# Kernel optimization log

Hardware: AMD Instinct MI355X
Metric: run time of the kernel (lower is better)

Reference implementation:

```python
import jax, jax.numpy as jnp
import numpy as np


def setup_inputs() -> dict:
    key = jax.random.key(0)
    ks = jax.random.split(key, 6)
    B, S, H, F, E = 4, 2048, 1024, 4096, 8
    x = jax.random.normal(ks[0], (B, S, H), dtype=jnp.float32)
    Wg = jax.random.normal(ks[1], (H, E), dtype=jnp.float32) * (1.0 / np.sqrt(H))
    W1 = jax.random.normal(ks[2], (E, H, F), dtype=jnp.float32) * (1.0 / np.sqrt(H))
    b1 = jnp.zeros((E, F), dtype=jnp.float32)
    W2 = jax.random.normal(ks[3], (E, F, H), dtype=jnp.float32) * (1.0 / np.sqrt(F))
    b2 = jnp.zeros((E, H), dtype=jnp.float32)
    return {"x": x, "Wg": Wg, "W1": W1, "b1": b1, "W2": W2, "b2": b2}


def _moe_forward(x, Wg, W1, b1, W2, b2):
    B, S, H = x.shape
    E = Wg.shape[1]
    tokens = x.reshape(-1, H)            # [T, H]
    T = tokens.shape[0]
    C = -(-T // E)                       # capacity = ceil(T/E), capacity_factor=1.0, min_capacity=0

    # --- top-1 gating (deepspeed top1gating) ---
    logits = tokens @ Wg                 # [T, E]
    gates = jax.nn.softmax(logits, axis=-1)
    idx = jnp.argmax(gates, axis=1)      # chosen expert per token
    mask1 = jax.nn.one_hot(idx, E, dtype=gates.dtype)          # [T, E]
    locations1 = jnp.cumsum(mask1, axis=0) - 1.0               # position within expert
    mask1 = mask1 * (locations1 < C).astype(gates.dtype)       # drop tokens over capacity
    loc_s = jnp.sum(locations1 * mask1, axis=1).astype(jnp.int32)  # [T]
    gates1 = jnp.sum(gates * mask1, axis=1)                    # [T] gate value (0 if dropped)

    # dispatch mask [T, E, C]: 1 at (token's expert, token's slot) if kept
    loc_oh = jax.nn.one_hot(loc_s, C, dtype=gates.dtype)       # [T, C]
    dispatch = mask1[:, :, None] * loc_oh[:, None, :]          # [T, E, C]
    combine = gates1[:, None, None] * dispatch                 # [T, E, C]

    # --- dispatch -> grouped expert MLP -> combine ---
    expert_in = jnp.einsum("tec,th->ech", dispatch, tokens)    # [E, C, H]
    hidden = jax.nn.relu(jnp.einsum("ech,ehf->ecf", expert_in, W1) + b1[:, None, :])
    expert_out = jnp.einsum("ecf,efh->ech", hidden, W2) + b2[:, None, :]
    out = jnp.einsum("tec,ech->th", combine, expert_out)       # [T, H]
    return out.reshape(B, S, H)


def reference(x, Wg, W1, b1, W2, b2):
    return _moe_forward(x, Wg, W1, b1, W2, b2)
```

## Files before the change

### kernel.cpp

```cpp
#include <hip/hip_runtime.h>
#include <hip/hip_bf16.h>
#include <hip/hip_fp16.h>

#define T_TOK 8192
#define HDIM  1024
#define FDIM  4096
#define NEXP  8
#define CAP   1024

typedef _Float16 f16x8 __attribute__((ext_vector_type(8)));
typedef float    f32x4 __attribute__((ext_vector_type(4)));

__device__ __forceinline__ unsigned short f2h_u(float f) {
    _Float16 h = (_Float16)f;
    return __builtin_bit_cast(unsigned short, h);
}

#define GLOAD_LDS16(gp, lp)                                                              \
    __builtin_amdgcn_global_load_lds((const __attribute__((address_space(1))) void*)(gp),\
                                     (__attribute__((address_space(3))) void*)(lp),      \
                                     16, 0, 0)

__global__ __launch_bounds__(256) void gate_kernel(const float* __restrict__ x,
                                                   const float* __restrict__ Wg,
                                                   int* __restrict__ eidx,
                                                   float* __restrict__ gate) {
    __shared__ float wgt[NEXP * HDIM];
    const int tid = threadIdx.x;
    for (int i = tid; i < NEXP * HDIM; i += 256) {
        int h = i >> 3, e = i & 7;
        wgt[e * HDIM + h] = Wg[i];
    }
    __syncthreads();
    const int lane = tid & 63;
    const int t = blockIdx.x * 4 + (tid >> 6);
    const float* xr = x + (size_t)t * HDIM;
    float acc[NEXP];
#pragma unroll
    for (int e = 0; e < NEXP; e++) acc[e] = 0.f;
    for (int h = lane; h < HDIM; h += 64) {
        float xv = xr[h];
#pragma unroll
        for (int e = 0; e < NEXP; e++) acc[e] += xv * wgt[e * HDIM + h];
    }
#pragma unroll
    for (int e = 0; e < NEXP; e++) {
#pragma unroll
        for (int s = 32; s > 0; s >>= 1) acc[e] += __shfl_xor(acc[e], s);
    }
    if (lane == 0) {
        float mx = acc[0]; int mi = 0;
#pragma unroll
        for (int e = 1; e < NEXP; e++) { if (acc[e] > mx) { mx = acc[e]; mi = e; } }
        float den = 0.f;
#pragma unroll
        for (int e = 0; e < NEXP; e++) den += expf(acc[e] - mx);
        eidx[t] = mi;
        gate[t] = 1.0f / den;
    }
}

__global__ __launch_bounds__(512) void scan_kernel(const int* __restrict__ eidx,
                                                   const float* __restrict__ gate,
                                                   int* __restrict__ tok,
                                                   float* __restrict__ gslot) {
    __shared__ int sidx[T_TOK];
    for (int i = threadIdx.x; i < T_TOK; i += 512) sidx[i] = eidx[i];
    __syncthreads();
    const int e = threadIdx.x >> 6, lane = threadIdx.x & 63;
    const unsigned long long below = (lane == 0) ? 0ull : (~0ull >> (64 - lane));
    int cnt = 0;
    for (int c0 = 0; c0 < T_TOK; c0 += 64) {
        int t = c0 + lane;
        int my = sidx[t];
        unsigned long long b = __ballot(my == e);
        if (my == e) {
            int pos = cnt + __popcll(b & below);
            if (pos < CAP) { tok[e * CAP + pos] = t; gslot[e * CAP + pos] = gate[t]; }
        }
        cnt += __popcll(b);
    }
}

__global__ __launch_bounds__(256) void gather_kernel(const float* __restrict__ x,
                                                     const int* __restrict__ tok,
                                                     unsigned short* __restrict__ A) {
    const int row = blockIdx.x;
    const int t = tok[row];
    unsigned short* dst = A + (size_t)row * HDIM;
    if (t < 0) {
        ushort4 z; z.x = z.y = z.z = z.w = 0;
        ((ushort4*)dst)[threadIdx.x] = z;
    } else {
        float4 v = ((const float4*)(x + (size_t)t * HDIM))[threadIdx.x];
        ushort4 o;
        o.x = f2h_u(v.x); o.y = f2h_u(v.y); o.z = f2h_u(v.z); o.w = f2h_u(v.w);
        ((ushort4*)dst)[threadIdx.x] = o;
    }
}

__global__ __launch_bounds__(256) void transpose_kernel(const float* __restrict__ in,
                                                        unsigned short* __restrict__ out,
                                                        int R, int Cdim) {
    __shared__ unsigned short tile[64][72];
    const int e = blockIdx.z;
    const size_t esz = (size_t)R * Cdim;
    const float* ine = in + e * esz;
    unsigned short* oute = out + e * esz;
    const int r0 = blockIdx.y * 64, c0 = blockIdx.x * 64;
    const int tid = threadIdx.x;
    const int rr = tid >> 4;
    const int c4 = (tid & 15) * 4;
#pragma unroll
    for (int rb = 0; rb < 64; rb += 16) {
        int r = rb + rr;
        float4 v = *(const float4*)&ine[(size_t)(r0 + r) * Cdim + c0 + c4];
        tile[c4 + 0][r] = f2h_u(v.x);
        tile[c4 + 1][r] = f2h_u(v.y);
        tile[c4 + 2][r] = f2h_u(v.z);
        tile[c4 + 3][r] = f2h_u(v.w);
    }
    __syncthreads();
    const int c = tid >> 2;
    const int rseg = (tid & 3) * 16;
    ushort4 o0 = *(const ushort4*)&tile[c][rseg + 0];
    ushort4 o1 = *(const ushort4*)&tile[c][rseg + 4];
    ushort4 o2 = *(const ushort4*)&tile[c][rseg + 8];
    ushort4 o3 = *(const ushort4*)&tile[c][rseg + 12];
    unsigned short* op = &oute[(size_t)(c0 + c) * R + r0 + rseg];
    ((ushort4*)op)[0] = o0; ((ushort4*)op)[1] = o1;
    ((ushort4*)op)[2] = o2; ((ushort4*)op)[3] = o3;
}

__global__ __launch_bounds__(256) void gemm1_kernel(const unsigned short* __restrict__ A,
                                                    const unsigned short* __restrict__ Bt,
                                                    const float* __restrict__ b1,
                                                    unsigned short* __restrict__ hid) {
    __shared__ __align__(16) unsigned short As[128 * 64];
    __shared__ __align__(16) unsigned short Bs[128 * 64];
    const int e = blockIdx.z;
    const int m0 = blockIdx.y * 128;
    const int n0 = blockIdx.x * 128;
    const int tid = threadIdx.x;
    const int lane = tid & 63;
    const int wr = ((tid >> 7) & 1) * 64;
    const int wc = ((tid >> 6) & 1) * 64;
    const unsigned short* Ae = A + ((size_t)e * CAP + m0) * HDIM;
    const unsigned short* Be = Bt + ((size_t)e * FDIM + n0) * HDIM;
    f32x4 acc[4][4];
    f32x4 zz = {0.f, 0.f, 0.f, 0.f};
#pragma unroll
    for (int i = 0; i < 4; i++)
#pragma unroll
        for (int j = 0; j < 4; j++) acc[i][j] = zz;

    const int srow = tid >> 3;
    const int sslot = tid & 7;
    for (int k0 = 0; k0 < HDIM; k0 += 64) {
#pragma unroll
        for (int j = 0; j < 4; j++) {
            int row = j * 32 + srow;
            int col = k0 + ((sslot ^ (row & 7)) << 3);
            GLOAD_LDS16(Ae + (size_t)row * HDIM + col, &As[(size_t)(j * 256 + tid) * 8]);
            GLOAD_LDS16(Be + (size_t)row * HDIM + col, &Bs[(size_t)(j * 256 + tid) * 8]);
        }
        __syncthreads();
#pragma unroll
        for (int ks = 0; ks < 2; ks++) {
            f16x8 af[4], bfr[4];
#pragma unroll
            for (int mi = 0; mi < 4; mi++) {
                int row = wr + mi * 16 + (lane & 15);
                int slotk = ks * 4 + (lane >> 4);
                af[mi] = *(const f16x8*)((const char*)As + row * 128 + ((slotk ^ (row & 7)) << 4));
            }
#pragma unroll
            for (int ni = 0; ni < 4; ni++) {
                int row = wc + ni * 16 + (lane & 15);
                int slotk = ks * 4 + (lane >> 4);
                bfr[ni] = *(const f16x8*)((const char*)Bs + row * 128 + ((slotk ^ (row & 7)) << 4));
            }
#pragma unroll
            for (int mi = 0; mi < 4; mi++)
#pragma unroll
                for (int ni = 0; ni < 4; ni++)
                    acc[mi][ni] = __builtin_amdgcn_mfma_f32_16x16x32_f16(af[mi], bfr[ni], acc[mi][ni], 0, 0, 0);
        }
        __syncthreads();
    }
    const int r4 = (lane >> 4) * 4;
#pragma unroll
    for (int ni = 0; ni < 4; ni++) {
        int col = n0 + wc + ni * 16 + (lane & 15);
        float bv = b1[e * FDIM + col];
#pragma unroll
        for (int mi = 0; mi < 4; mi++) {
#pragma unroll
            for (int j = 0; j < 4; j++) {
                int row = m0 + wr + mi * 16 + r4 + j;
                float v = acc[mi][ni][j] + bv;
                hid[((size_t)e * CAP + row) * FDIM + col] = f2h_u(v > 0.f ? v : 0.f);
            }
        }
    }
}

__global__ __launch_bounds__(256) void gemm2_kernel(const unsigned short* __restrict__ A,
                                                    const unsigned short* __restrict__ Bt,
                                                    const float* __restrict__ b2,
                                                    const int* __restrict__ tok,
                                                    const float* __restrict__ gslot,
                                                    float* __restrict__ out) {
    __shared__ __align__(16) unsigned short As[128 * 64];
    __shared__ __align__(16) unsigned short Bs[128 * 64];
    __shared__ int ts[128];
    __shared__ float sg[128];
    const int e = blockIdx.z;
    const int m0 = blockIdx.y * 128;
    const int n0 = blockIdx.x * 128;
    const int tid = threadIdx.x;
    if (tid < 128) {
        int t = tok[e * CAP + m0 + tid];
        ts[tid] = t;
        sg[tid] = (t >= 0) ? gslot[e * CAP + m0 + tid] : 0.f;
    }
    const int lane = tid & 63;
    const int wr = ((tid >> 7) & 1) * 64;
    const int wc = ((tid >> 6) & 1) * 64;
    const unsigned short* Ae = A + ((size_t)e * CAP + m0) * FDIM;
    const unsigned short* Be = Bt + ((size_t)e * HDIM + n0) * FDIM;
    f32x4 acc[4][4];
    f32x4 zz = {0.f, 0.f, 0.f, 0.f};
#pragma unroll
    for (int i = 0; i < 4; i++)
#pragma unroll
        for (int j = 0; j < 4; j++) acc[i][j] = zz;

    const int srow = tid >> 3;
    const int sslot = tid & 7;
    for (int k0 = 0; k0 < FDIM; k0 += 64) {
#pragma unroll
        for (int j = 0; j < 4; j++) {
            int row = j * 32 + srow;
            int col = k0 + ((sslot ^ (row & 7)) << 3);
            GLOAD_LDS16(Ae + (size_t)row * FDIM + col, &As[(size_t)(j * 256 + tid) * 8]);
            GLOAD_LDS16(Be + (size_t)row * FDIM + col, &Bs[(size_t)(j * 256 + tid) * 8]);
        }
        __syncthreads();
#pragma unroll
        for (int ks = 0; ks < 2; ks++) {
            f16x8 af[4], bfr[4];
#pragma unroll
            for (int mi = 0; mi < 4; mi++) {
                int row = wr + mi * 16 + (lane & 15);
                int slotk = ks * 4 + (lane >> 4);
                af[mi] = *(const f16x8*)((const char*)As + row * 128 + ((slotk ^ (row & 7)) << 4));
            }
#pragma unroll
            for (int ni = 0; ni < 4; ni++) {
                int row = wc + ni * 16 + (lane & 15);
                int slotk = ks * 4 + (lane >> 4);
                bfr[ni] = *(const f16x8*)((const char*)Bs + row * 128 + ((slotk ^ (row & 7)) << 4));
            }
#pragma unroll
            for (int mi = 0; mi < 4; mi++)
#pragma unroll
                for (int ni = 0; ni < 4; ni++)
                    acc[mi][ni] = __builtin_amdgcn_mfma_f32_16x16x32_f16(af[mi], bfr[ni], acc[mi][ni], 0, 0, 0);
        }
        __syncthreads();
    }
    const int r4 = (lane >> 4) * 4;
#pragma unroll
    for (int ni = 0; ni < 4; ni++) {
        int col = n0 + wc + ni * 16 + (lane & 15);
        float bv = b2[e * HDIM + col];
#pragma unroll
        for (int mi = 0; mi < 4; mi++) {
#pragma unroll
            for (int j = 0; j < 4; j++) {
                int rl = wr + mi * 16 + r4 + j;
                int t = ts[rl];
                if (t >= 0)
                    out[(size_t)t * HDIM + col] = sg[rl] * (acc[mi][ni][j] + bv);
            }
        }
    }
}

extern "C" void kernel_launch(void* const* d_in, const int* in_sizes, int n_in,
                              void* d_out, int out_size, void* d_ws, size_t ws_size,
                              hipStream_t stream) {
    const float* x  = (const float*)d_in[0];
    const float* Wg = (const float*)d_in[1];
    const float* W1 = (const float*)d_in[2];
    const float* b1 = (const float*)d_in[3];
    const float* W2 = (const float*)d_in[4];
    const float* b2 = (const float*)d_in[5];
    float* out = (float*)d_out;

    char* ws = (char*)d_ws;
    const size_t SMALL   = 128 * 1024;
    const size_t A_BYTES = (size_t)T_TOK * HDIM * 2;
    const size_t H_BYTES = (size_t)T_TOK * FDIM * 2;
    const size_t W_BYTES = (size_t)NEXP * HDIM * FDIM * 2;

    int*   eidx = (int*)(ws);
    float* gate = (float*)(ws + 32 * 1024);
    int*   tok  = (int*)(ws + 64 * 1024);
    float* gsl  = (float*)(ws + 96 * 1024);
    unsigned short* Abuf = (unsigned short*)(ws + SMALL);
    unsigned short* Hbuf = (unsigned short*)(ws + SMALL + A_BYTES);
    unsigned short* Wt1  = (unsigned short*)(ws + SMALL + A_BYTES + H_BYTES);
    const int two_buf = (ws_size >= SMALL + A_BYTES + H_BYTES + 2 * W_BYTES);
    unsigned short* Wt2 = two_buf ? (Wt1 + W_BYTES / 2) : Wt1;

    hipMemsetAsync(d_out, 0, (size_t)T_TOK * HDIM * 4, stream);
    hipMemsetAsync(tok, 0xFF, NEXP * CAP * 4, stream);

    transpose_kernel<<<dim3(FDIM / 64, HDIM / 64, NEXP), 256, 0, stream>>>(W1, Wt1, HDIM, FDIM);
    if (two_buf)
        transpose_kernel<<<dim3(HDIM / 64, FDIM / 64, NEXP), 256, 0, stream>>>(W2, Wt2, FDIM, HDIM);

    gate_kernel<<<T_TOK / 4, 256, 0, stream>>>(x, Wg, eidx, gate);
    scan_kernel<<<1, 512, 0, stream>>>(eidx, gate, tok, gsl);
    gather_kernel<<<NEXP * CAP, 256, 0, stream>>>(x, tok, Abuf);

    gemm1_kernel<<<dim3(FDIM / 128, CAP / 128, NEXP), 256, 0, stream>>>(Abuf, Wt1, b1, Hbuf);

    if (!two_buf)
        transpose_kernel<<<dim3(HDIM / 64, FDIM / 64, NEXP), 256, 0, stream>>>(W2, Wt2, FDIM, HDIM);

    gemm2_kernel<<<dim3(HDIM / 128, CAP / 128, NEXP), 256, 0, stream>>>(Hbuf, Wt2, b2, tok, gsl, out);
}
```

Baseline: 629.0 us.

## Double-buffer GEMM LDS tiles and merge weight transposes into one kernel

Both expert GEMMs now use two LDS buffers, so the async global-to-LDS load of the next K tile is issued before the MFMAs on the current tile run, with one barrier per iteration instead of two. The two weight transpose launches are merged into a single kernel that uses larger 256x64 tiles and writes 16-byte vectors. The aim is to hide global load latency behind compute and to make the fp32-to-fp16 weight conversion more bandwidth-efficient. LDS use per GEMM block doubles to 64KB, which may reduce occupancy.

```diff
diff --git a/kernel.cpp b/kernel.cpp
--- a/kernel.cpp
+++ b/kernel.cpp
@@ -10,6 +10,7 @@
 
 typedef _Float16 f16x8 __attribute__((ext_vector_type(8)));
 typedef float    f32x4 __attribute__((ext_vector_type(4)));
+typedef unsigned short u16x8 __attribute__((ext_vector_type(8)));
 
 __device__ __forceinline__ unsigned short f2h_u(float f) {
     _Float16 h = (_Float16)f;
@@ -99,45 +100,57 @@
     }
 }
 
-__global__ __launch_bounds__(256) void transpose_kernel(const float* __restrict__ in,
-                                                        unsigned short* __restrict__ out,
-                                                        int R, int Cdim) {
-    __shared__ unsigned short tile[64][72];
-    const int e = blockIdx.z;
-    const size_t esz = (size_t)R * Cdim;
-    const float* ine = in + e * esz;
-    unsigned short* oute = out + e * esz;
-    const int r0 = blockIdx.y * 64, c0 = blockIdx.x * 64;
+#define TR_PAD 264
+__global__ __launch_bounds__(256) void wtrans_kernel(const float* __restrict__ W1,
+                                                     const float* __restrict__ W2,
+                                                     unsigned short* __restrict__ Wt1,
+                                                     unsigned short* __restrict__ Wt2,
+                                                     int w1_tiles) {
+    __shared__ unsigned short tile[64][TR_PAD];
+    const int bid = blockIdx.x;
+    const float* in; unsigned short* out; int R, C;
+    int e, cx, ry;
+    if (bid < w1_tiles) {
+        e = bid >> 8; int rem = bid & 255;
+        cx = rem & 63; ry = rem >> 6;
+        in = W1 + (size_t)e * HDIM * FDIM; out = Wt1 + (size_t)e * HDIM * FDIM;
+        R = HDIM; C = FDIM;
+    } else {
+        int b = bid - w1_tiles;
+        e = b >> 8; int rem = b & 255;
+        cx = rem & 15; ry = rem >> 4;
+        in = W2 + (size_t)e * HDIM * FDIM; out = Wt2 + (size_t)e * HDIM * FDIM;
+        R = FDIM; C = HDIM;
+    }
+    const int r0 = ry * 256, c0 = cx * 64;
     const int tid = threadIdx.x;
-    const int rr = tid >> 4;
-    const int c4 = (tid & 15) * 4;
-#pragma unroll
-    for (int rb = 0; rb < 64; rb += 16) {
-        int r = rb + rr;
-        float4 v = *(const float4*)&ine[(size_t)(r0 + r) * Cdim + c0 + c4];
+    const int rr = tid >> 4, c4 = (tid & 15) * 4;
+#pragma unroll
+    for (int p = 0; p < 16; p++) {
+        int r = p * 16 + rr;
+        float4 v = *(const float4*)&in[(size_t)(r0 + r) * C + c0 + c4];
         tile[c4 + 0][r] = f2h_u(v.x);
         tile[c4 + 1][r] = f2h_u(v.y);
         tile[c4 + 2][r] = f2h_u(v.z);
         tile[c4 + 3][r] = f2h_u(v.w);
     }
     __syncthreads();
-    const int c = tid >> 2;
-    const int rseg = (tid & 3) * 16;
-    ushort4 o0 = *(const ushort4*)&tile[c][rseg + 0];
-    ushort4 o1 = *(const ushort4*)&tile[c][rseg + 4];
-    ushort4 o2 = *(const ushort4*)&tile[c][rseg + 8];
-    ushort4 o3 = *(const ushort4*)&tile[c][rseg + 12];
-    unsigned short* op = &oute[(size_t)(c0 + c) * R + r0 + rseg];
-    ((ushort4*)op)[0] = o0; ((ushort4*)op)[1] = o1;
-    ((ushort4*)op)[2] = o2; ((ushort4*)op)[3] = o3;
+    const int cc = tid >> 5;
+    const int rc = (tid & 31) * 8;
+#pragma unroll
+    for (int p = 0; p < 8; p++) {
+        int c = p * 8 + cc;
+        u16x8 v = *(const u16x8*)&tile[c][rc];
+        *(u16x8*)&out[(size_t)(c0 + c) * R + r0 + rc] = v;
+    }
 }
 
 __global__ __launch_bounds__(256) void gemm1_kernel(const unsigned short* __restrict__ A,
                                                     const unsigned short* __restrict__ Bt,
                                                     const float* __restrict__ b1,
                                                     unsigned short* __restrict__ hid) {
-    __shared__ __align__(16) unsigned short As[128 * 64];
-    __shared__ __align__(16) unsigned short Bs[128 * 64];
+    __shared__ __align__(16) unsigned short As[2][128 * 64];
+    __shared__ __align__(16) unsigned short Bs[2][128 * 64];
     const int e = blockIdx.z;
     const int m0 = blockIdx.y * 128;
     const int n0 = blockIdx.x * 128;
@@ -156,15 +169,16 @@
 
     const int srow = tid >> 3;
     const int sslot = tid & 7;
-    for (int k0 = 0; k0 < HDIM; k0 += 64) {
+    auto stage = [&](int buf, int k0) {
 #pragma unroll
         for (int j = 0; j < 4; j++) {
             int row = j * 32 + srow;
             int col = k0 + ((sslot ^ (row & 7)) << 3);
-            GLOAD_LDS16(Ae + (size_t)row * HDIM + col, &As[(size_t)(j * 256 + tid) * 8]);
-            GLOAD_LDS16(Be + (size_t)row * HDIM + col, &Bs[(size_t)(j * 256 + tid) * 8]);
-        }
-        __syncthreads();
+            GLOAD_LDS16(Ae + (size_t)row * HDIM + col, &As[buf][(j * 256 + tid) * 8]);
+            GLOAD_LDS16(Be + (size_t)row * HDIM + col, &Bs[buf][(j * 256 + tid) * 8]);
+        }
+    };
+    auto compute = [&](int buf) {
 #pragma unroll
         for (int ks = 0; ks < 2; ks++) {
             f16x8 af[4], bfr[4];
@@ -172,13 +186,13 @@
             for (int mi = 0; mi < 4; mi++) {
                 int row = wr + mi * 16 + (lane & 15);
                 int slotk = ks * 4 + (lane >> 4);
-                af[mi] = *(const f16x8*)((const char*)As + row * 128 + ((slotk ^ (row & 7)) << 4));
+                af[mi] = *(const f16x8*)((const char*)&As[buf][0] + row * 128 + ((slotk ^ (row & 7)) << 4));
             }
 #pragma unroll
             for (int ni = 0; ni < 4; ni++) {
                 int row = wc + ni * 16 + (lane & 15);
                 int slotk = ks * 4 + (lane >> 4);
-                bfr[ni] = *(const f16x8*)((const char*)Bs + row * 128 + ((slotk ^ (row & 7)) << 4));
+                bfr[ni] = *(const f16x8*)((const char*)&Bs[buf][0] + row * 128 + ((slotk ^ (row & 7)) << 4));
             }
 #pragma unroll
             for (int mi = 0; mi < 4; mi++)
@@ -186,8 +200,19 @@
                 for (int ni = 0; ni < 4; ni++)
                     acc[mi][ni] = __builtin_amdgcn_mfma_f32_16x16x32_f16(af[mi], bfr[ni], acc[mi][ni], 0, 0, 0);
         }
+    };
+
+    stage(0, 0);
+    __syncthreads();
+    int cur = 0;
+    for (int k0 = 64; k0 < HDIM; k0 += 64) {
+        stage(cur ^ 1, k0);
+        compute(cur);
         __syncthreads();
-    }
+        cur ^= 1;
+    }
+    compute(cur);
+
     const int r4 = (lane >> 4) * 4;
 #pragma unroll
     for (int ni = 0; ni < 4; ni++) {
@@ -211,8 +236,8 @@
                                                     const int* __restrict__ tok,
                                                     const float* __restrict__ gslot,
                                                     float* __restrict__ out) {
-    __shared__ __align__(16) unsigned short As[128 * 64];
-    __shared__ __align__(16) unsigned short Bs[128 * 64];
+    __shared__ __align__(16) unsigned short As[2][128 * 64];
+    __shared__ __align__(16) unsigned short Bs[2][128 * 64];
     __shared__ int ts[128];
     __shared__ float sg[128];
     const int e = blockIdx.z;
@@ -238,15 +263,16 @@
 
     const int srow = tid >> 3;
     const int sslot = tid & 7;
-    for (int k0 = 0; k0 < FDIM; k0 += 64) {
+    auto stage = [&](int buf, int k0) {
 #pragma unroll
         for (int j = 0; j < 4; j++) {
             int row = j * 32 + srow;
             int col = k0 + ((sslot ^ (row & 7)) << 3);
-            GLOAD_LDS16(Ae + (size_t)row * FDIM + col, &As[(size_t)(j * 256 + tid) * 8]);
-            GLOAD_LDS16(Be + (size_t)row * FDIM + col, &Bs[(size_t)(j * 256 + tid) * 8]);
-        }
-        __syncthreads();
+            GLOAD_LDS16(Ae + (size_t)row * FDIM + col, &As[buf][(j * 256 + tid) * 8]);
+            GLOAD_LDS16(Be + (size_t)row * FDIM + col, &Bs[buf][(j * 256 + tid) * 8]);
+        }
+    };
+    auto compute = [&](int buf) {
 #pragma unroll
         for (int ks = 0; ks < 2; ks++) {
             f16x8 af[4], bfr[4];
@@ -254,13 +280,13 @@
             for (int mi = 0; mi < 4; mi++) {
                 int row = wr + mi * 16 + (lane & 15);
                 int slotk = ks * 4 + (lane >> 4);
-                af[mi] = *(const f16x8*)((const char*)As + row * 128 + ((slotk ^ (row & 7)) << 4));
+                af[mi] = *(const f16x8*)((const char*)&As[buf][0] + row * 128 + ((slotk ^ (row & 7)) << 4));
             }
 #pragma unroll
             for (int ni = 0; ni < 4; ni++) {
                 int row = wc + ni * 16 + (lane & 15);
                 int slotk = ks * 4 + (lane >> 4);
-                bfr[ni] = *(const f16x8*)((const char*)Bs + row * 128 + ((slotk ^ (row & 7)) << 4));
+                bfr[ni] = *(const f16x8*)((const char*)&Bs[buf][0] + row * 128 + ((slotk ^ (row & 7)) << 4));
             }
 #pragma unroll
             for (int mi = 0; mi < 4; mi++)
@@ -268,8 +294,19 @@
                 for (int ni = 0; ni < 4; ni++)
                     acc[mi][ni] = __builtin_amdgcn_mfma_f32_16x16x32_f16(af[mi], bfr[ni], acc[mi][ni], 0, 0, 0);
         }
+    };
+
+    stage(0, 0);
+    __syncthreads();
+    int cur = 0;
+    for (int k0 = 64; k0 < FDIM; k0 += 64) {
+        stage(cur ^ 1, k0);
+        compute(cur);
         __syncthreads();
-    }
+        cur ^= 1;
+    }
+    compute(cur);
+
     const int r4 = (lane >> 4) * 4;
 #pragma unroll
     for (int ni = 0; ni < 4; ni++) {
@@ -318,9 +355,11 @@
     hipMemsetAsync(d_out, 0, (size_t)T_TOK * HDIM * 4, stream);
     hipMemsetAsync(tok, 0xFF, NEXP * CAP * 4, stream);
 
-    transpose_kernel<<<dim3(FDIM / 64, HDIM / 64, NEXP), 256, 0, stream>>>(W1, Wt1, HDIM, FDIM);
-    if (two_buf)
-        transpose_kernel<<<dim3(HDIM / 64, FDIM / 64, NEXP), 256, 0, stream>>>(W2, Wt2, FDIM, HDIM);
+    if (two_buf) {
+        wtrans_kernel<<<4096, 256, 0, stream>>>(W1, W2, Wt1, Wt2, 2048);
+    } else {
+        wtrans_kernel<<<2048, 256, 0, stream>>>(W1, W2, Wt1, Wt2, 2048);
+    }
 
     gate_kernel<<<T_TOK / 4, 256, 0, stream>>>(x, Wg, eidx, gate);
     scan_kernel<<<1, 512, 0, stream>>>(eidx, gate, tok, gsl);
@@ -329,7 +368,7 @@
     gemm1_kernel<<<dim3(FDIM / 128, CAP / 128, NEXP), 256, 0, stream>>>(Abuf, Wt1, b1, Hbuf);
 
     if (!two_buf)
-        transpose_kernel<<<dim3(HDIM / 64, FDIM / 64, NEXP), 256, 0, stream>>>(W2, Wt2, FDIM, HDIM);
+        wtrans_kernel<<<2048, 256, 0, stream>>>(W1, W2, Wt1, Wt2, 0);
 
     gemm2_kernel<<<dim3(HDIM / 128, CAP / 128, NEXP), 256, 0, stream>>>(Hbuf, Wt2, b2, tok, gsl, out);
 }
```

After: 684.8 us. +8.9%, slower.
